# Performance work log

Measured on AMD Instinct MI355X. Metric: run time of the kernel, lower is better.

## Reference

```python
import jax, jax.numpy as jnp
import numpy as np

# pool sizes (must match init_kwargs)
N_FQK, N_FV, N_REL, N_VAL, N_KNOW = 512, 256, 128, 32, 256
K_FQK, K_FV, K_REL, K_VAL = 64, 32, 16, 3
D_MODEL, D_SPACE = 1024, 64
B, S = 8, 2048


def _topk_sparsify(w, k):
    # keep top-k entries per row, zero the rest (values unchanged)
    vals, idx = jax.lax.top_k(w, k)                      # [B,k]
    out = jnp.zeros_like(w)
    rows = jnp.arange(w.shape[0])[:, None]
    return out.at[rows, idx].set(vals), idx


def setup_inputs() -> dict:
    key = jax.random.key(0)
    k1, k2, k3, k4 = jax.random.split(key, 4)
    x = jax.random.normal(k1, (B, S, D_MODEL), dtype=jnp.float32)
    # importance: per-token weights normalized over sequence
    importance = jax.nn.softmax(jax.random.normal(k2, (B, S), dtype=jnp.float32), axis=-1)
    W = jax.random.normal(k3, (D_MODEL, D_SPACE), dtype=jnp.float32) * 0.02
    b = jnp.zeros((D_SPACE,), dtype=jnp.float32)
    total = N_FQK + N_FV + N_REL + N_VAL + N_KNOW
    neuron_emb = jax.random.normal(k4, (total, D_SPACE), dtype=jnp.float32) * 0.02
    return {"x": x, "importance": importance, "W": W, "b": b, "neuron_emb": neuron_emb}


def reference(x, importance, W, b, neuron_emb):
    # projection (dropout inactive in eval); normalized neuron embeddings
    h = x @ W + b                                         # [B,S,d_space]
    emb_n = neuron_emb / jnp.linalg.norm(neuron_emb, axis=-1, keepdims=True)
    all_logits = jnp.einsum('bsd,nd->bsn', h, emb_n)      # [B,S,N_total]

    e0 = N_FQK
    e1 = e0 + N_FV
    e2 = e1 + N_REL
    e3 = e2 + N_VAL

    def route(lo, hi):
        pref = jax.nn.softmax(all_logits[..., lo:hi], axis=-1)  # [B,S,n]
        w = jnp.einsum('bs,bsn->bn', importance, pref)          # [B,n]
        return pref, w

    _, w_qk = route(0, e0)
    _, idx_qk = jax.lax.top_k(w_qk, K_FQK)
    idx_qk = jnp.sort(idx_qk, axis=-1)

    _, w_v = route(e0, e1)
    _, idx_v = jax.lax.top_k(w_v, K_FV)
    idx_v = jnp.sort(idx_v, axis=-1)

    # relational Q and K share the same logit slice (eval: no excitability bonus)
    _, w_rQ = route(e1, e2)
    _, w_rK = route(e1, e2)
    rw_Q, _ = _topk_sparsify(w_rQ, K_REL)
    rw_K, _ = _topk_sparsify(w_rK, K_REL)

    _, w_val = route(e2, e3)
    vw, _ = _topk_sparsify(w_val, K_VAL)

    return idx_qk, idx_v, rw_Q, rw_K, vw, w_qk, w_v
```

## Files before the change

kernel.cpp:

```cpp
#include <hip/hip_runtime.h>
#include <hip/hip_bf16.h>
#include <hip/hip_fp16.h>
#include <math.h>

#define ROWS  16384
#define DM    1024
#define DS    64
#define NUSE  928
#define NPAD  960
#define NT    15

typedef __attribute__((ext_vector_type(8))) short bf16x8;
typedef __attribute__((ext_vector_type(4))) float f32x4;

static __device__ inline f32x4 mfma16(bf16x8 a, bf16x8 b, f32x4 c) {
    return __builtin_amdgcn_mfma_f32_16x16x32_bf16(a, b, c, 0, 0, 0);
}

static __device__ inline void bfsplit(float v, unsigned short& h, unsigned short& l) {
    unsigned u = __float_as_uint(v);
    unsigned hr = u + 0x7FFFu + ((u >> 16) & 1u);
    h = (unsigned short)(hr >> 16);
    float hf = __uint_as_float((unsigned)h << 16);
    float r = v - hf;
    unsigned ur = __float_as_uint(r);
    unsigned lr2 = ur + 0x7FFFu + ((ur >> 16) & 1u);
    l = (unsigned short)(lr2 >> 16);
}

#define OFF_EBH  0LL
#define OFF_EBL  122880LL
#define OFF_WBH  245760LL
#define OFF_WBL  376832LL
#define OFF_WP   507904LL

__global__ __launch_bounds__(256) void k_prep(const float* __restrict__ emb,
                                              const float* __restrict__ W,
                                              unsigned short* __restrict__ ebh,
                                              unsigned short* __restrict__ ebl,
                                              unsigned short* __restrict__ wbh,
                                              unsigned short* __restrict__ wbl) {
    if (blockIdx.x < 4) {
        int n = blockIdx.x * 256 + threadIdx.x;
        if (n >= NPAD) return;
        if (n >= NUSE) {
            #pragma unroll
            for (int d = 0; d < DS; d++) {
                int kt = d >> 5, q = (d >> 3) & 3, j = d & 7;
                int a = ((kt * 4 + q) * NPAD + n) * 8 + j;
                ebh[a] = 0; ebl[a] = 0;
            }
            return;
        }
        float ss = 0.f;
        #pragma unroll
        for (int d = 0; d < DS; d++) { float v = emb[n * DS + d]; ss = fmaf(v, v, ss); }
        float inv = 1.0f / sqrtf(ss);
        #pragma unroll
        for (int d = 0; d < DS; d++) {
            float v = emb[n * DS + d] * inv;
            unsigned short h, l; bfsplit(v, h, l);
            int kt = d >> 5, q = (d >> 3) & 3, j = d & 7;
            int a = ((kt * 4 + q) * NPAD + n) * 8 + j;
            ebh[a] = h; ebl[a] = l;
        }
    } else {
        int idx = (blockIdx.x - 4) * 256 + threadIdx.x;
        int ktg = idx >> 6, n = idx & 63;
        #pragma unroll
        for (int q = 0; q < 4; q++) {
            #pragma unroll
            for (int j = 0; j < 8; j++) {
                int k = ktg * 32 + q * 8 + j;
                float v = W[k * DS + n];
                unsigned short h, l; bfsplit(v, h, l);
                int a = ((ktg * 4 + q) * 64 + n) * 8 + j;
                wbh[a] = h; wbl[a] = l;
            }
        }
    }
}

__global__ __launch_bounds__(1024, 4) void k_mega(const float* __restrict__ x,
                                                  const float* __restrict__ bias,
                                                  const unsigned short* __restrict__ wbh,
                                                  const unsigned short* __restrict__ wbl,
                                                  const unsigned short* __restrict__ ebh,
                                                  const unsigned short* __restrict__ ebl,
                                                  const float* __restrict__ imp,
                                                  float* __restrict__ wpart) {
    __shared__ __align__(16) unsigned char smem[159744];
    unsigned short* Ph = (unsigned short*)smem;
    unsigned short* Xh = (unsigned short*)smem;
    unsigned short* Xl = (unsigned short*)(smem + 16384);
    unsigned short* Hh = (unsigned short*)(smem + 138240);
    unsigned short* Hl = (unsigned short*)(smem + 146432);
    float* zslot = (float*)(smem + 154624);
    float* coefL = (float*)(smem + 158720);

    const int tid = threadIdx.x;
    const int rc = blockIdx.x;
    const long long row0 = (long long)rc * 64;

    zslot[tid & 1023] = 0.f;

    const int w = tid >> 6, lane = tid & 63, q = lane >> 4, lm = lane & 15;

    const int rg = w >> 2, cg = w & 3;
    const int sr = tid >> 4, ss = tid & 15;
    const float* xrow = &x[(row0 + sr) * DM + ss * 8];
    const int skt = ss >> 2, sq = ss & 3;
    const int sbase = ((skt * 4 + sq) * 64 + sr) * 8;

    f32x4 hacc;
    hacc.x = 0.f; hacc.y = 0.f; hacc.z = 0.f; hacc.w = 0.f;

    float4 pf0 = *(const float4*)&xrow[0];
    float4 pf1 = *(const float4*)&xrow[4];

    for (int ch = 0; ch < 8; ch++) {
        if (ch) __syncthreads();
        {
            unsigned short h0, l0, h1, l1, h2, l2, h3, l3;
            bfsplit(pf0.x, h0, l0); bfsplit(pf0.y, h1, l1);
            bfsplit(pf0.z, h2, l2); bfsplit(pf0.w, h3, l3);
            uint2 ph; ph.x = (unsigned)h0 | ((unsigned)h1 << 16); ph.y = (unsigned)h2 | ((unsigned)h3 << 16);
            uint2 pl; pl.x = (unsigned)l0 | ((unsigned)l1 << 16); pl.y = (unsigned)l2 | ((unsigned)l3 << 16);
            *(uint2*)&Xh[sbase] = ph;
            *(uint2*)&Xl[sbase] = pl;
            bfsplit(pf1.x, h0, l0); bfsplit(pf1.y, h1, l1);
            bfsplit(pf1.z, h2, l2); bfsplit(pf1.w, h3, l3);
            ph.x = (unsigned)h0 | ((unsigned)h1 << 16); ph.y = (unsigned)h2 | ((unsigned)h3 << 16);
            pl.x = (unsigned)l0 | ((unsigned)l1 << 16); pl.y = (unsigned)l2 | ((unsigned)l3 << 16);
            *(uint2*)&Xh[sbase + 4] = ph;
            *(uint2*)&Xl[sbase + 4] = pl;
        }
        if (ch < 7) {
            pf0 = *(const float4*)&xrow[(ch + 1) * 128];
            pf1 = *(const float4*)&xrow[(ch + 1) * 128 + 4];
        }
        __syncthreads();
        #pragma unroll
        for (int kt = 0; kt < 4; kt++) {
            const bf16x8 a_h = *(const bf16x8*)&Xh[((kt * 4 + q) * 64 + rg * 16 + lm) * 8];
            const bf16x8 a_l = *(const bf16x8*)&Xl[((kt * 4 + q) * 64 + rg * 16 + lm) * 8];
            const int ktg = ch * 4 + kt;
            const int ba = ((ktg * 4 + q) * 64 + cg * 16 + lm) * 8;
            const bf16x8 b_h = *(const bf16x8*)&wbh[ba];
            const bf16x8 b_l = *(const bf16x8*)&wbl[ba];
            hacc = mfma16(a_h, b_h, hacc);
            hacc = mfma16(a_h, b_l, hacc);
            hacc = mfma16(a_l, b_h, hacc);
        }
    }
    __syncthreads();

    {
        const int D = cg * 16 + lm;
        const float bv = bias[D];
        const int ktD = D >> 5, qD = (D >> 3) & 3, jD = D & 7;
        #pragma unroll
        for (int t = 0; t < 4; t++) {
            const int R = rg * 16 + q * 4 + t;
            float v = hacc[t] + bv;
            unsigned short hh, ll; bfsplit(v, hh, ll);
            Hh[((ktD * 4 + qD) * 64 + R) * 8 + jD] = hh;
            Hl[((ktD * 4 + qD) * 64 + R) * 8 + jD] = ll;
        }
    }
    __syncthreads();

    const int rw = w & 3, wg = w >> 2;

    bf16x8 a_h[2], a_l[2];
    #pragma unroll
    for (int kt = 0; kt < 2; kt++) {
        int ab = ((kt * 4 + q) * 64 + rw * 16 + lm) * 8;
        a_h[kt] = *(const bf16x8*)&Hh[ab];
        a_l[kt] = *(const bf16x8*)&Hl[ab];
    }

    #pragma unroll
    for (int v = 0; v < 4; v++) {
        int nt = wg + v * 4;
        if (nt > 14) continue;
        f32x4 acc[4];
        #pragma unroll
        for (int f = 0; f < 4; f++) { acc[f].x = 0.f; acc[f].y = 0.f; acc[f].z = 0.f; acc[f].w = 0.f; }
        #pragma unroll
        for (int kt = 0; kt < 2; kt++) {
            #pragma unroll
            for (int f = 0; f < 4; f++) {
                int bb = ((kt * 4 + q) * NPAD + nt * 64 + f * 16 + lm) * 8;
                bf16x8 b_h = *(const bf16x8*)&ebh[bb];
                bf16x8 b_l = *(const bf16x8*)&ebl[bb];
                acc[f] = mfma16(a_h[kt], b_h, acc[f]);
                acc[f] = mfma16(a_h[kt], b_l, acc[f]);
                acc[f] = mfma16(a_l[kt], b_h, acc[f]);
            }
        }
        const int sl = (nt < 8) ? 0 : (nt < 12) ? 1 : (nt < 14) ? 2 : 3;
        float s0 = 0.f, s1 = 0.f, s2 = 0.f, s3 = 0.f;
        #pragma unroll
        for (int f = 0; f < 4; f++) {
            float e0 = __expf(acc[f][0]);
            float e1 = __expf(acc[f][1]);
            float e2 = __expf(acc[f][2]);
            float e3 = __expf(acc[f][3]);
            int n = nt * 64 + f * 16 + lm;
            unsigned short p0 = __half_as_ushort(__float2half(e0));
            unsigned short p1 = __half_as_ushort(__float2half(e1));
            unsigned short p2 = __half_as_ushort(__float2half(e2));
            unsigned short p3 = __half_as_ushort(__float2half(e3));
            uint2 pk; pk.x = (unsigned)p0 | ((unsigned)p1 << 16); pk.y = (unsigned)p2 | ((unsigned)p3 << 16);
            *(uint2*)&Ph[n * 72 + rw * 16 + q * 4] = pk;
            if (nt * 64 + f * 16 < NUSE) {
                s0 += e0; s1 += e1; s2 += e2; s3 += e3;
            }
        }
        #pragma unroll
        for (int off = 1; off < 16; off <<= 1) {
            s0 += __shfl_xor(s0, off); s1 += __shfl_xor(s1, off);
            s2 += __shfl_xor(s2, off); s3 += __shfl_xor(s3, off);
        }
        if (lm < 4) {
            float sv = (lm == 0) ? s0 : (lm == 1) ? s1 : (lm == 2) ? s2 : s3;
            zslot[(wg * 4 + sl) * 64 + rw * 16 + q * 4 + lm] += sv;
        }
    }
    __syncthreads();

    if (tid < 64) {
        int r = tid;
        float im = imp[rc * 64 + r];
        #pragma unroll
        for (int sl = 0; sl < 4; sl++) {
            float Z = zslot[(0 * 4 + sl) * 64 + r] + zslot[(1 * 4 + sl) * 64 + r]
                    + zslot[(2 * 4 + sl) * 64 + r] + zslot[(3 * 4 + sl) * 64 + r];
            coefL[r * 4 + sl] = im / Z;
        }
    }
    __syncthreads();

    if (tid < NUSE) {
        int n = tid;
        int sl = (n < 512) ? 0 : (n < 768) ? 1 : (n < 896) ? 2 : 3;
        float acc = 0.f;
        #pragma unroll
        for (int rb = 0; rb < 8; rb++) {
            uint4 pk = *(const uint4*)&Ph[n * 72 + rb * 8];
            const unsigned pv[4] = {pk.x, pk.y, pk.z, pk.w};
            #pragma unroll
            for (int u = 0; u < 4; u++) {
                float v0 = __half2float(__ushort_as_half((unsigned short)(pv[u] & 0xFFFF)));
                float v1 = __half2float(__ushort_as_half((unsigned short)(pv[u] >> 16)));
                int row = rb * 8 + u * 2;
                acc = fmaf(coefL[(row + 0) * 4 + sl], v0, acc);
                acc = fmaf(coefL[(row + 1) * 4 + sl], v1, acc);
            }
        }
        wpart[(long long)rc * NPAD + n] = acc;
    }
}

__global__ __launch_bounds__(512) void k_out(const float* __restrict__ wpart,
                                             float* __restrict__ out) {
    const int b = blockIdx.x;
    const int tid = threadIdx.x;
    __shared__ float w_s[NUSE];
    __shared__ int   rk[NUSE];

    for (int n = tid; n < NUSE; n += 512) {
        float s = 0.f;
        #pragma unroll 4
        for (int c = 0; c < 32; c++)
            s += wpart[(long long)(b * 32 + c) * NPAD + n];
        w_s[n] = s;
        if (n < 512)      out[3072 + (long long)b * 512 + n] = s;
        else if (n < 768) out[7168 + (long long)b * 256 + (n - 512)] = s;
    }
    __syncthreads();

    for (int n = tid; n < NUSE; n += 512) {
        int lo, hi;
        if (n < 512)      { lo = 0;   hi = 512; }
        else if (n < 768) { lo = 512; hi = 768; }
        else if (n < 896) { lo = 768; hi = 896; }
        else              { lo = 896; hi = NUSE; }
        float wn = w_s[n];
        int r = 0;
        for (int m = lo; m < hi; m++) {
            float wm = w_s[m];
            r += (wm > wn) || ((wm == wn) && (m < n));
        }
        rk[n] = r;
    }
    __syncthreads();

    if (tid < 512) {
        int n = tid;
        if (rk[n] < 64) {
            int pos = 0;
            for (int m = 0; m < n; m++) pos += (rk[m] < 64) ? 1 : 0;
            out[(long long)b * 64 + pos] = (float)n;
        }
    }
    if (tid < 256) {
        int n = 512 + tid;
        if (rk[n] < 32) {
            int pos = 0;
            for (int m = 512; m < n; m++) pos += (rk[m] < 32) ? 1 : 0;
            out[512 + (long long)b * 32 + pos] = (float)tid;
        }
    }
    if (tid < 128) {
        int n = 768 + tid;
        float v = (rk[n] < 16) ? w_s[n] : 0.f;
        out[768 + (long long)b * 128 + tid] = v;
        out[1792 + (long long)b * 128 + tid] = v;
    }
    if (tid < 32) {
        int n = 896 + tid;
        float v = (rk[n] < 3) ? w_s[n] : 0.f;
        out[2816 + (long long)b * 32 + tid] = v;
    }
}

extern "C" void kernel_launch(void* const* d_in, const int* in_sizes, int n_in,
                              void* d_out, int out_size, void* d_ws, size_t ws_size,
                              hipStream_t stream) {
    const float* x    = (const float*)d_in[0];
    const float* imp  = (const float*)d_in[1];
    const float* W    = (const float*)d_in[2];
    const float* bias = (const float*)d_in[3];
    const float* emb  = (const float*)d_in[4];

    char* ws = (char*)d_ws;
    unsigned short* ebh = (unsigned short*)(ws + OFF_EBH);
    unsigned short* ebl = (unsigned short*)(ws + OFF_EBL);
    unsigned short* wbh = (unsigned short*)(ws + OFF_WBH);
    unsigned short* wbl = (unsigned short*)(ws + OFF_WBL);
    float* wpart        = (float*)(ws + OFF_WP);
    float* out          = (float*)d_out;

    k_prep<<<12, 256, 0, stream>>>(emb, W, ebh, ebl, wbh, wbl);
    k_mega<<<256, 1024, 0, stream>>>(x, bias, wbh, wbl, ebh, ebl, imp, wpart);
    k_out<<<8, 512, 0, stream>>>(wpart, out);
}
```

Baseline: 158.6 us.

## Split K across waves with direct x loads and halve row tile per block

The mega kernel now handles 32 rows per block with 512 threads and launches 512 blocks instead of 256 blocks of 1024 threads, so more blocks cover the CUs. The x projection no longer stages x through shared memory. Each wave loads its x slice straight from global into registers, computes a split-K partial over a quarter of D_MODEL, and the partials are reduced through shared memory. This drops the per-chunk barriers and LDS staging, cuts shared memory use, and gives better occupancy. The cost is twice as many partial rows for k_out to reduce and extra LDS traffic for the split-K reduction.

Measured after the change: 169.5 us. 1.07x slower.

```diff
diff --git a/kernel.cpp b/kernel.cpp
--- a/kernel.cpp
+++ b/kernel.cpp
@@ -81,108 +81,99 @@
     }
 }
 
-__global__ __launch_bounds__(1024, 4) void k_mega(const float* __restrict__ x,
-                                                  const float* __restrict__ bias,
-                                                  const unsigned short* __restrict__ wbh,
-                                                  const unsigned short* __restrict__ wbl,
-                                                  const unsigned short* __restrict__ ebh,
-                                                  const unsigned short* __restrict__ ebl,
-                                                  const float* __restrict__ imp,
-                                                  float* __restrict__ wpart) {
-    __shared__ __align__(16) unsigned char smem[159744];
+__global__ __launch_bounds__(512, 4) void k_mega(const float* __restrict__ x,
+                                                 const float* __restrict__ bias,
+                                                 const unsigned short* __restrict__ wbh,
+                                                 const unsigned short* __restrict__ wbl,
+                                                 const unsigned short* __restrict__ ebh,
+                                                 const unsigned short* __restrict__ ebl,
+                                                 const float* __restrict__ imp,
+                                                 float* __restrict__ wpart) {
+    __shared__ __align__(16) unsigned char smem[79872];
     unsigned short* Ph = (unsigned short*)smem;
-    unsigned short* Xh = (unsigned short*)smem;
-    unsigned short* Xl = (unsigned short*)(smem + 16384);
-    unsigned short* Hh = (unsigned short*)(smem + 138240);
-    unsigned short* Hl = (unsigned short*)(smem + 146432);
-    float* zslot = (float*)(smem + 154624);
-    float* coefL = (float*)(smem + 158720);
+    float* Cbuf = (float*)smem;
+    unsigned short* Hh = (unsigned short*)(smem + 69120);
+    unsigned short* Hl = (unsigned short*)(smem + 73216);
+    float* zslot = (float*)(smem + 77312);
+    float* coefL = (float*)(smem + 79360);
 
     const int tid = threadIdx.x;
     const int rc = blockIdx.x;
-    const long long row0 = (long long)rc * 64;
-
-    zslot[tid & 1023] = 0.f;
-
+    const long long row0 = (long long)rc * 32;
     const int w = tid >> 6, lane = tid & 63, q = lane >> 4, lm = lane & 15;
 
-    const int rg = w >> 2, cg = w & 3;
-    const int sr = tid >> 4, ss = tid & 15;
-    const float* xrow = &x[(row0 + sr) * DM + ss * 8];
-    const int skt = ss >> 2, sq = ss & 3;
-    const int sbase = ((skt * 4 + sq) * 64 + sr) * 8;
-
-    f32x4 hacc;
-    hacc.x = 0.f; hacc.y = 0.f; hacc.z = 0.f; hacc.w = 0.f;
-
-    float4 pf0 = *(const float4*)&xrow[0];
-    float4 pf1 = *(const float4*)&xrow[4];
-
-    for (int ch = 0; ch < 8; ch++) {
-        if (ch) __syncthreads();
-        {
-            unsigned short h0, l0, h1, l1, h2, l2, h3, l3;
-            bfsplit(pf0.x, h0, l0); bfsplit(pf0.y, h1, l1);
-            bfsplit(pf0.z, h2, l2); bfsplit(pf0.w, h3, l3);
-            uint2 ph; ph.x = (unsigned)h0 | ((unsigned)h1 << 16); ph.y = (unsigned)h2 | ((unsigned)h3 << 16);
-            uint2 pl; pl.x = (unsigned)l0 | ((unsigned)l1 << 16); pl.y = (unsigned)l2 | ((unsigned)l3 << 16);
-            *(uint2*)&Xh[sbase] = ph;
-            *(uint2*)&Xl[sbase] = pl;
-            bfsplit(pf1.x, h0, l0); bfsplit(pf1.y, h1, l1);
-            bfsplit(pf1.z, h2, l2); bfsplit(pf1.w, h3, l3);
-            ph.x = (unsigned)h0 | ((unsigned)h1 << 16); ph.y = (unsigned)h2 | ((unsigned)h3 << 16);
-            pl.x = (unsigned)l0 | ((unsigned)l1 << 16); pl.y = (unsigned)l2 | ((unsigned)l3 << 16);
-            *(uint2*)&Xh[sbase + 4] = ph;
-            *(uint2*)&Xl[sbase + 4] = pl;
-        }
-        if (ch < 7) {
-            pf0 = *(const float4*)&xrow[(ch + 1) * 128];
-            pf1 = *(const float4*)&xrow[(ch + 1) * 128 + 4];
+    zslot[tid] = 0.f;
+
+    const int rg = w >> 2, kg = w & 3;
+    {
+        const float* xp = &x[(row0 + rg * 16 + lm) * (long long)DM + kg * 256 + q * 8];
+        f32x4 acc[4];
+        #pragma unroll
+        for (int f = 0; f < 4; f++) { acc[f].x = 0.f; acc[f].y = 0.f; acc[f].z = 0.f; acc[f].w = 0.f; }
+
+        #pragma unroll
+        for (int ks = 0; ks < 8; ks++) {
+            float4 v0 = *(const float4*)&xp[ks * 32];
+            float4 v1 = *(const float4*)&xp[ks * 32 + 4];
+            union { bf16x8 v; unsigned short s[8]; } ah, al;
+            bfsplit(v0.x, ah.s[0], al.s[0]); bfsplit(v0.y, ah.s[1], al.s[1]);
+            bfsplit(v0.z, ah.s[2], al.s[2]); bfsplit(v0.w, ah.s[3], al.s[3]);
+            bfsplit(v1.x, ah.s[4], al.s[4]); bfsplit(v1.y, ah.s[5], al.s[5]);
+            bfsplit(v1.z, ah.s[6], al.s[6]); bfsplit(v1.w, ah.s[7], al.s[7]);
+            const int ktg = kg * 8 + ks;
+            #pragma unroll
+            for (int f = 0; f < 4; f++) {
+                const int ba = ((ktg * 4 + q) * 64 + f * 16 + lm) * 8;
+                const bf16x8 b_h = *(const bf16x8*)&wbh[ba];
+                const bf16x8 b_l = *(const bf16x8*)&wbl[ba];
+                acc[f] = mfma16(ah.v, b_h, acc[f]);
+                acc[f] = mfma16(ah.v, b_l, acc[f]);
+                acc[f] = mfma16(al.v, b_h, acc[f]);
+            }
+        }
+        #pragma unroll
+        for (int f = 0; f < 4; f++)
+            #pragma unroll
+            for (int t = 0; t < 4; t++)
+                Cbuf[w * 1088 + (q * 4 + t) * 68 + f * 16 + lm] = acc[f][t];
+    }
+    __syncthreads();
+
+    {
+        const int r = tid >> 4, seg = tid & 15;
+        const int rgg = r >> 4, rl = r & 15;
+        const int c0 = seg * 4;
+        float4 s = *(const float4*)&bias[c0];
+        #pragma unroll
+        for (int g = 0; g < 4; g++) {
+            float4 a = *(const float4*)&Cbuf[(rgg * 4 + g) * 1088 + rl * 68 + c0];
+            s.x += a.x; s.y += a.y; s.z += a.z; s.w += a.w;
         }
         __syncthreads();
-        #pragma unroll
-        for (int kt = 0; kt < 4; kt++) {
-            const bf16x8 a_h = *(const bf16x8*)&Xh[((kt * 4 + q) * 64 + rg * 16 + lm) * 8];
-            const bf16x8 a_l = *(const bf16x8*)&Xl[((kt * 4 + q) * 64 + rg * 16 + lm) * 8];
-            const int ktg = ch * 4 + kt;
-            const int ba = ((ktg * 4 + q) * 64 + cg * 16 + lm) * 8;
-            const bf16x8 b_h = *(const bf16x8*)&wbh[ba];
-            const bf16x8 b_l = *(const bf16x8*)&wbl[ba];
-            hacc = mfma16(a_h, b_h, hacc);
-            hacc = mfma16(a_h, b_l, hacc);
-            hacc = mfma16(a_l, b_h, hacc);
-        }
-    }
-    __syncthreads();
-
-    {
-        const int D = cg * 16 + lm;
-        const float bv = bias[D];
-        const int ktD = D >> 5, qD = (D >> 3) & 3, jD = D & 7;
-        #pragma unroll
-        for (int t = 0; t < 4; t++) {
-            const int R = rg * 16 + q * 4 + t;
-            float v = hacc[t] + bv;
-            unsigned short hh, ll; bfsplit(v, hh, ll);
-            Hh[((ktD * 4 + qD) * 64 + R) * 8 + jD] = hh;
-            Hl[((ktD * 4 + qD) * 64 + R) * 8 + jD] = ll;
-        }
-    }
-    __syncthreads();
-
-    const int rw = w & 3, wg = w >> 2;
-
+        unsigned short h0, l0, h1, l1, h2, l2, h3, l3;
+        bfsplit(s.x, h0, l0); bfsplit(s.y, h1, l1);
+        bfsplit(s.z, h2, l2); bfsplit(s.w, h3, l3);
+        const int ktH = c0 >> 5, qH = (c0 >> 3) & 3, jH = c0 & 7;
+        const int base = ((ktH * 4 + qH) * 32 + r) * 8 + jH;
+        uint2 ph; ph.x = (unsigned)h0 | ((unsigned)h1 << 16); ph.y = (unsigned)h2 | ((unsigned)h3 << 16);
+        uint2 pl; pl.x = (unsigned)l0 | ((unsigned)l1 << 16); pl.y = (unsigned)l2 | ((unsigned)l3 << 16);
+        *(uint2*)&Hh[base] = ph;
+        *(uint2*)&Hl[base] = pl;
+    }
+    __syncthreads();
+
+    const int wg = w & 3, rgp = w >> 2;
     bf16x8 a_h[2], a_l[2];
     #pragma unroll
     for (int kt = 0; kt < 2; kt++) {
-        int ab = ((kt * 4 + q) * 64 + rw * 16 + lm) * 8;
+        const int ab = ((kt * 4 + q) * 32 + rgp * 16 + lm) * 8;
         a_h[kt] = *(const bf16x8*)&Hh[ab];
         a_l[kt] = *(const bf16x8*)&Hl[ab];
     }
 
     #pragma unroll
     for (int v = 0; v < 4; v++) {
-        int nt = wg + v * 4;
+        const int nt = wg + v * 4;
         if (nt > 14) continue;
         f32x4 acc[4];
         #pragma unroll
@@ -191,9 +182,9 @@
         for (int kt = 0; kt < 2; kt++) {
             #pragma unroll
             for (int f = 0; f < 4; f++) {
-                int bb = ((kt * 4 + q) * NPAD + nt * 64 + f * 16 + lm) * 8;
-                bf16x8 b_h = *(const bf16x8*)&ebh[bb];
-                bf16x8 b_l = *(const bf16x8*)&ebl[bb];
+                const int bb = ((kt * 4 + q) * NPAD + nt * 64 + f * 16 + lm) * 8;
+                const bf16x8 b_h = *(const bf16x8*)&ebh[bb];
+                const bf16x8 b_l = *(const bf16x8*)&ebl[bb];
                 acc[f] = mfma16(a_h[kt], b_h, acc[f]);
                 acc[f] = mfma16(a_h[kt], b_l, acc[f]);
                 acc[f] = mfma16(a_l[kt], b_h, acc[f]);
@@ -207,13 +198,13 @@
             float e1 = __expf(acc[f][1]);
             float e2 = __expf(acc[f][2]);
             float e3 = __expf(acc[f][3]);
-            int n = nt * 64 + f * 16 + lm;
+            const int n = nt * 64 + f * 16 + lm;
             unsigned short p0 = __half_as_ushort(__float2half(e0));
             unsigned short p1 = __half_as_ushort(__float2half(e1));
             unsigned short p2 = __half_as_ushort(__float2half(e2));
             unsigned short p3 = __half_as_ushort(__float2half(e3));
             uint2 pk; pk.x = (unsigned)p0 | ((unsigned)p1 << 16); pk.y = (unsigned)p2 | ((unsigned)p3 << 16);
-            *(uint2*)&Ph[n * 72 + rw * 16 + q * 4] = pk;
+            *(uint2*)&Ph[n * 36 + rgp * 16 + q * 4] = pk;
             if (nt * 64 + f * 16 < NUSE) {
                 s0 += e0; s1 += e1; s2 += e2; s3 += e3;
             }
@@ -225,41 +216,40 @@
         }
         if (lm < 4) {
             float sv = (lm == 0) ? s0 : (lm == 1) ? s1 : (lm == 2) ? s2 : s3;
-            zslot[(wg * 4 + sl) * 64 + rw * 16 + q * 4 + lm] += sv;
-        }
-    }
-    __syncthreads();
-
-    if (tid < 64) {
-        int r = tid;
-        float im = imp[rc * 64 + r];
+            zslot[(wg * 4 + sl) * 32 + rgp * 16 + q * 4 + lm] += sv;
+        }
+    }
+    __syncthreads();
+
+    if (tid < 32) {
+        const int r = tid;
+        const float im = imp[row0 + r];
         #pragma unroll
         for (int sl = 0; sl < 4; sl++) {
-            float Z = zslot[(0 * 4 + sl) * 64 + r] + zslot[(1 * 4 + sl) * 64 + r]
-                    + zslot[(2 * 4 + sl) * 64 + r] + zslot[(3 * 4 + sl) * 64 + r];
+            float Z = zslot[(0 * 4 + sl) * 32 + r] + zslot[(1 * 4 + sl) * 32 + r]
+                    + zslot[(2 * 4 + sl) * 32 + r] + zslot[(3 * 4 + sl) * 32 + r];
             coefL[r * 4 + sl] = im / Z;
         }
     }
     __syncthreads();
 
-    if (tid < NUSE) {
-        int n = tid;
-        int sl = (n < 512) ? 0 : (n < 768) ? 1 : (n < 896) ? 2 : 3;
+    for (int nn = tid; nn < NUSE; nn += 512) {
+        const int sl = (nn < 512) ? 0 : (nn < 768) ? 1 : (nn < 896) ? 2 : 3;
         float acc = 0.f;
         #pragma unroll
         for (int rb = 0; rb < 8; rb++) {
-            uint4 pk = *(const uint4*)&Ph[n * 72 + rb * 8];
-            const unsigned pv[4] = {pk.x, pk.y, pk.z, pk.w};
-            #pragma unroll
-            for (int u = 0; u < 4; u++) {
-                float v0 = __half2float(__ushort_as_half((unsigned short)(pv[u] & 0xFFFF)));
-                float v1 = __half2float(__ushort_as_half((unsigned short)(pv[u] >> 16)));
-                int row = rb * 8 + u * 2;
-                acc = fmaf(coefL[(row + 0) * 4 + sl], v0, acc);
-                acc = fmaf(coefL[(row + 1) * 4 + sl], v1, acc);
-            }
-        }
-        wpart[(long long)rc * NPAD + n] = acc;
+            uint2 pk = *(const uint2*)&Ph[nn * 36 + rb * 4];
+            float v0 = __half2float(__ushort_as_half((unsigned short)(pk.x & 0xFFFF)));
+            float v1 = __half2float(__ushort_as_half((unsigned short)(pk.x >> 16)));
+            float v2 = __half2float(__ushort_as_half((unsigned short)(pk.y & 0xFFFF)));
+            float v3 = __half2float(__ushort_as_half((unsigned short)(pk.y >> 16)));
+            const int row = rb * 4;
+            acc = fmaf(coefL[(row + 0) * 4 + sl], v0, acc);
+            acc = fmaf(coefL[(row + 1) * 4 + sl], v1, acc);
+            acc = fmaf(coefL[(row + 2) * 4 + sl], v2, acc);
+            acc = fmaf(coefL[(row + 3) * 4 + sl], v3, acc);
+        }
+        wpart[(long long)rc * NPAD + nn] = acc;
     }
 }
 
@@ -273,8 +263,8 @@
     for (int n = tid; n < NUSE; n += 512) {
         float s = 0.f;
         #pragma unroll 4
-        for (int c = 0; c < 32; c++)
-            s += wpart[(long long)(b * 32 + c) * NPAD + n];
+        for (int c = 0; c < 64; c++)
+            s += wpart[(long long)(b * 64 + c) * NPAD + n];
         w_s[n] = s;
         if (n < 512)      out[3072 + (long long)b * 512 + n] = s;
         else if (n < 768) out[7168 + (long long)b * 256 + (n - 512)] = s;
@@ -344,6 +334,6 @@
     float* out          = (float*)d_out;
 
     k_prep<<<12, 256, 0, stream>>>(emb, W, ebh, ebl, wbh, wbl);
-    k_mega<<<256, 1024, 0, stream>>>(x, bias, wbh, wbl, ebh, ebl, imp, wpart);
+    k_mega<<<512, 512, 0, stream>>>(x, bias, wbh, wbl, ebh, ebl, imp, wpart);
     k_out<<<8, 512, 0, stream>>>(wpart, out);
 }
```
